# Kernel optimization log

Measured on AMD Instinct MI355X. Metric: run time of the kernel, lower is better.

The kernel has to match this reference:

```python
import jax, jax.numpy as jnp
import numpy as np

H = W = 56
WS = 7            # window size
SHIFT = 3
HEADS = 6
DIM = 192
N = WS * WS       # tokens per window (49)
NW = (H // WS) * (W // WS)  # windows per image (64)
EPS = 1e-5


def _rel_pos_index():
    coords = np.stack(np.meshgrid(np.arange(WS), np.arange(WS), indexing='ij'))
    cf = coords.reshape(2, -1)
    rel = (cf[:, :, None] - cf[:, None, :]).transpose(1, 2, 0)
    rel[:, :, 0] += WS - 1
    rel[:, :, 1] += WS - 1
    rel[:, :, 0] *= 2 * WS - 1
    return rel.sum(-1).astype(np.int32)  # [N, N]


def _attn_mask():
    img = np.zeros([1, H, W, 1], dtype=np.float32)
    slices = (slice(0, -WS), slice(-WS, -SHIFT), slice(-SHIFT, None))
    cnt = 0
    for hs in slices:
        for ws_ in slices:
            img[:, hs, ws_, :] = cnt
            cnt += 1
    m = img.reshape(1, H // WS, WS, W // WS, WS, 1).transpose(0, 1, 3, 2, 4, 5)
    m = m.reshape(-1, N)                      # [nW, N]
    diff = m[:, None, :] - m[:, :, None]
    return np.where(diff != 0, -100.0, 0.0).astype(np.float32)  # [nW, N, N]

_RPI = _rel_pos_index()
_MASK = _attn_mask()


def _ln(x, g, b):
    mu = jnp.mean(x, axis=-1, keepdims=True)
    var = jnp.mean(jnp.square(x - mu), axis=-1, keepdims=True)
    return (x - mu) * jax.lax.rsqrt(var + EPS) * g + b


def setup_inputs() -> dict:
    key = jax.random.key(0)
    ks = jax.random.split(key, 12)
    C, Hd = DIM, DIM * 4
    s = lambda n: 1.0 / np.sqrt(n)
    return {
        'x': jax.random.normal(ks[0], (32, H * W, C), jnp.float32),
        'norm1_g': jnp.ones((C,), jnp.float32),
        'norm1_b': jnp.zeros((C,), jnp.float32),
        'qkv_w': jax.random.normal(ks[1], (C, 3 * C), jnp.float32) * s(C),
        'qkv_b': jnp.zeros((3 * C,), jnp.float32),
        'bias_table': jax.random.normal(ks[2], ((2 * WS - 1) ** 2, HEADS), jnp.float32) * 0.02,
        'proj_w': jax.random.normal(ks[3], (C, C), jnp.float32) * s(C),
        'proj_b': jnp.zeros((C,), jnp.float32),
        'norm2_g': jnp.ones((C,), jnp.float32),
        'norm2_b': jnp.zeros((C,), jnp.float32),
        'fc1_w': jax.random.normal(ks[4], (C, Hd), jnp.float32) * s(C),
        'fc1_b': jnp.zeros((Hd,), jnp.float32),
        'fc2_w': jax.random.normal(ks[5], (Hd, C), jnp.float32) * s(Hd),
        'fc2_b': jnp.zeros((C,), jnp.float32),
    }


def reference(x, norm1_g, norm1_b, qkv_w, qkv_b, bias_table, proj_w, proj_b,
              norm2_g, norm2_b, fc1_w, fc1_b, fc2_w, fc2_b):
    B, L, C = x.shape
    hd = C // HEADS
    scale = hd ** -0.5

    shortcut = x
    h = _ln(x, norm1_g, norm1_b).reshape(B, H, W, C)
    h = jnp.roll(h, (-SHIFT, -SHIFT), axis=(1, 2))

    # window partition -> [B*nW, N, C]
    h = h.reshape(B, H // WS, WS, W // WS, WS, C).transpose(0, 1, 3, 2, 4, 5)
    xw = h.reshape(B * NW, N, C)

    qkv = (xw @ qkv_w + qkv_b).reshape(B * NW, N, 3, HEADS, hd)
    q, k, v = jnp.moveaxis(qkv, 2, 0)                 # each [B*nW, N, H, d]
    q = jnp.swapaxes(q, 1, 2) * scale                 # [B*nW, H, N, d]
    k = jnp.swapaxes(k, 1, 2)
    v = jnp.swapaxes(v, 1, 2)

    attn = jnp.einsum('whnd,whmd->whnm', q, k)        # [B*nW, H, N, N]
    bias = bias_table[jnp.asarray(_RPI).reshape(-1)].reshape(N, N, HEADS)
    attn = attn + jnp.transpose(bias, (2, 0, 1))[None]
    mask = jnp.asarray(_MASK)                         # [nW, N, N]
    attn = attn.reshape(B, NW, HEADS, N, N) + mask[None, :, None]
    attn = jax.nn.softmax(attn.reshape(B * NW, HEADS, N, N), axis=-1)

    out = jnp.einsum('whnm,whmd->whnd', attn, v)      # [B*nW, H, N, d]
    out = jnp.swapaxes(out, 1, 2).reshape(B * NW, N, C)
    out = out @ proj_w + proj_b

    # window reverse -> [B, H, W, C]
    out = out.reshape(B, H // WS, W // WS, WS, WS, C).transpose(0, 1, 3, 2, 4, 5)
    out = out.reshape(B, H, W, C)
    out = jnp.roll(out, (SHIFT, SHIFT), axis=(1, 2)).reshape(B, L, C)

    x = shortcut + out
    hmlp = _ln(x, norm2_g, norm2_b)
    hmlp = jax.nn.gelu(hmlp @ fc1_w + fc1_b, approximate=False) @ fc2_w + fc2_b
    return x + hmlp
```

## Files before the change

### kernel.cpp

```cpp
#include <hip/hip_runtime.h>
#include <hip/hip_bf16.h>
#include <math.h>

static constexpr int CB     = 32;
static constexpr int CH     = 56;
static constexpr int CW     = 56;
static constexpr int CC     = 192;
static constexpr int CSHIFT = 3;
static constexpr int CN     = 49;
static constexpr int CNW    = 64;
static constexpr int CL     = CH * CW;
static constexpr int CM     = CB * CNW * CN;
static constexpr int CHID   = 768;
static constexpr int LN1_BLOCKS  = CM / 4;
static constexpr int PREP_TOTAL  = 110592 + 36864 + 147456 + 147456 + 98304;
static constexpr int PREP_BLOCKS = (PREP_TOTAL + 255) / 256;

typedef __attribute__((ext_vector_type(8))) __bf16 bf16x8;
typedef __attribute__((ext_vector_type(4))) float  f32x4;

__device__ __forceinline__ float bfu2f(unsigned short u) {
  union { unsigned i; float f; } c; c.i = (unsigned)u << 16; return c.f;
}
__device__ __forceinline__ unsigned short f2bu(float f) {
  __hip_bfloat16 b = __float2bfloat16(f);
  return *(unsigned short*)&b;
}
__device__ __forceinline__ float gelu_fast(float v) {
  float e = __expf(-1.702f * v);
  return __fdividef(v, 1.0f + e);
}

#define GLOAD16(g, l) __builtin_amdgcn_global_load_lds( \
    (__attribute__((address_space(1))) void*)(g),       \
    (__attribute__((address_space(3))) void*)(l), 16, 0, 0)

__global__ __launch_bounds__(256)
void ln1_prep_kernel(const float* __restrict__ xin, const float* __restrict__ gamma,
                     const float* __restrict__ beta, __hip_bfloat16* __restrict__ out,
                     const float* __restrict__ qkv_w, const float* __restrict__ proj_w,
                     const float* __restrict__ fc1_w, const float* __restrict__ fc2_w,
                     const float* __restrict__ btab,
                     __hip_bfloat16* __restrict__ wq, __hip_bfloat16* __restrict__ wp,
                     __hip_bfloat16* __restrict__ w1, __hip_bfloat16* __restrict__ w2,
                     float* __restrict__ bias2)
{
  if (blockIdx.x < LN1_BLOCKS) {
    const int wid = threadIdx.x >> 6, lane = threadIdx.x & 63;
    const int m = blockIdx.x * 4 + wid;
    int b   = m / (CNW * CN);
    int rem = m - b * (CNW * CN);
    int nw  = rem / CN, t = rem - nw * CN;
    int wr = nw >> 3, wc = nw & 7;
    int ti = t / 7, tj = t - ti * 7;
    int sr = wr * 7 + ti + CSHIFT; if (sr >= CH) sr -= CH;
    int sc = wc * 7 + tj + CSHIFT; if (sc >= CW) sc -= CW;
    size_t src = ((size_t)b * CL + (size_t)sr * CW + sc) * CC;
    float v0 = xin[src + lane], v1 = xin[src + lane + 64], v2 = xin[src + lane + 128];
    float s  = v0 + v1 + v2;
    float sq = v0 * v0 + v1 * v1 + v2 * v2;
    #pragma unroll
    for (int off = 32; off; off >>= 1) { s += __shfl_xor(s, off); sq += __shfl_xor(sq, off); }
    const float mu  = s * (1.0f / CC);
    const float inv = rsqrtf(sq * (1.0f / CC) - mu * mu + 1e-5f);
    const size_t dst = (size_t)m * CC;
    out[dst + lane      ] = __float2bfloat16((v0 - mu) * inv * gamma[lane      ] + beta[lane      ]);
    out[dst + lane + 64 ] = __float2bfloat16((v1 - mu) * inv * gamma[lane + 64 ] + beta[lane + 64 ]);
    out[dst + lane + 128] = __float2bfloat16((v2 - mu) * inv * gamma[lane + 128] + beta[lane + 128]);
    return;
  }

  int idx = (blockIdx.x - LN1_BLOCKS) * 256 + threadIdx.x;
  if (idx < 110592) {
    int k = idx / 576, n = idx - k * 576;
    wq[n * 192 + k] = __float2bfloat16(qkv_w[idx]);
    return;
  }
  idx -= 110592;
  if (idx < 36864) {
    int k = idx / 192, n = idx - k * 192;
    wp[n * 192 + k] = __float2bfloat16(proj_w[idx]);
    return;
  }
  idx -= 36864;
  if (idx < 147456) {
    int k = idx / 768, n = idx - k * 768;
    w1[n * 192 + k] = __float2bfloat16(fc1_w[idx]);
    return;
  }
  idx -= 147456;
  if (idx < 147456) {
    int k = idx / 192, n = idx - k * 192;
    w2[n * 768 + k] = __float2bfloat16(fc2_w[idx]);
    return;
  }
  idx -= 147456;
  if (idx < 98304) {
    int j = idx & 63, i = (idx >> 6) & 63;
    int rest = idx >> 12;
    int h = rest % 6, wt = rest / 6;
    float val;
    if (i >= 49 || j >= 49) {
      val = -INFINITY;
    } else {
      int ti = i / 7, ci = i - ti * 7;
      int tj = j / 7, cj = j - tj * 7;
      val = btab[((ti - tj + 6) * 13 + (ci - cj + 6)) * 6 + h];
      int hri = (wt & 2) ? ((ti < 4) ? 1 : 2) : 0;
      int hci = (wt & 1) ? ((ci < 4) ? 1 : 2) : 0;
      int hrj = (wt & 2) ? ((tj < 4) ? 1 : 2) : 0;
      int hcj = (wt & 1) ? ((cj < 4) ? 1 : 2) : 0;
      if (hri * 3 + hci != hrj * 3 + hcj) val -= 100.0f;
    }
    bias2[idx] = val;
  }
}

__global__ __launch_bounds__(256)
void ln_kernel(const __hip_bfloat16* __restrict__ xin, const float* __restrict__ gamma,
               const float* __restrict__ beta, __hip_bfloat16* __restrict__ out)
{
  const int wid = threadIdx.x >> 6, lane = threadIdx.x & 63;
  const int m = blockIdx.x * 4 + wid;
  const size_t src = (size_t)m * CC;
  const unsigned short* xb = (const unsigned short*)xin;
  float v0 = bfu2f(xb[src + lane      ]);
  float v1 = bfu2f(xb[src + lane + 64 ]);
  float v2 = bfu2f(xb[src + lane + 128]);
  float s  = v0 + v1 + v2;
  float sq = v0 * v0 + v1 * v1 + v2 * v2;
  #pragma unroll
  for (int off = 32; off; off >>= 1) { s += __shfl_xor(s, off); sq += __shfl_xor(sq, off); }
  const float mu  = s * (1.0f / CC);
  const float inv = rsqrtf(sq * (1.0f / CC) - mu * mu + 1e-5f);
  out[src + lane      ] = __float2bfloat16((v0 - mu) * inv * gamma[lane      ] + beta[lane      ]);
  out[src + lane + 64 ] = __float2bfloat16((v1 - mu) * inv * gamma[lane + 64 ] + beta[lane + 64 ]);
  out[src + lane + 128] = __float2bfloat16((v2 - mu) * inv * gamma[lane + 128] + beta[lane + 128]);
}

template<int K, int N, int BN, int MODE>
__global__ __launch_bounds__(256)
void gemm_mfma(const __hip_bfloat16* __restrict__ Ain, const __hip_bfloat16* __restrict__ Wt,
               const float* __restrict__ bias, void* __restrict__ Outv,
               const void* __restrict__ residv)
{
  constexpr int NT = BN / 32;
  __shared__ short As[128 * 64];
  __shared__ short Bs[BN * 64];

  const int tid  = threadIdx.x;
  const int lane = tid & 63, wid = tid >> 6;

  const int nbx = N / BN;
  const int nwg = nbx * gridDim.y;
  const int wg  = blockIdx.y * nbx + blockIdx.x;
  const int swz = (wg & 7) * (nwg >> 3) + (wg >> 3);
  const int row0 = (swz / nbx) * 128, col0 = (swz % nbx) * BN;

  const int wm = wid >> 1, wn = wid & 1;
  const int lr = lane & 15, lg = lane >> 4;

  const short* A  = (const short*)Ain;
  const short* W  = (const short*)Wt;

  f32x4 acc[4][NT] = {};

  #pragma unroll
  for (int kk = 0; kk < K; kk += 64) {
    #pragma unroll
    for (int it = 0; it < 4; ++it) {
      int c = it * 256 + tid;
      int row = c >> 3, slot = c & 7;
      int kg = (slot ^ (row & 7)) * 8;
      GLOAD16(A + (size_t)(row0 + row) * K + kk + kg, As + c * 8);
    }
    #pragma unroll
    for (int it = 0; it < BN / 32; ++it) {
      int c = it * 256 + tid;
      int row = c >> 3, slot = c & 7;
      int kg = (slot ^ (row & 7)) * 8;
      GLOAD16(W + (size_t)(col0 + row) * K + kk + kg, Bs + c * 8);
    }
    __syncthreads();

    #pragma unroll
    for (int kh = 0; kh < 2; ++kh) {
      const int sb = kh * 4 + lg;
      bf16x8 bfr[NT];
      #pragma unroll
      for (int nt = 0; nt < NT; ++nt) {
        int br = wn * (BN / 2) + nt * 16 + lr;
        bfr[nt] = *(const bf16x8*)(Bs + br * 64 + (sb ^ (br & 7)) * 8);
      }
      #pragma unroll
      for (int m = 0; m < 4; ++m) {
        int ar = wm * 64 + m * 16 + lr;
        bf16x8 afr = *(const bf16x8*)(As + ar * 64 + (sb ^ (ar & 7)) * 8);
        #pragma unroll
        for (int nt = 0; nt < NT; ++nt)
          acc[m][nt] = __builtin_amdgcn_mfma_f32_16x16x32_bf16(afr, bfr[nt], acc[m][nt], 0, 0, 0);
      }
    }
    __syncthreads();
  }

  const int colA = col0 + wn * (BN / 2) + lr;
  float bv[NT];
  #pragma unroll
  for (int nt = 0; nt < NT; ++nt) bv[nt] = bias[colA + nt * 16];

  #pragma unroll
  for (int m = 0; m < 4; ++m) {
    #pragma unroll
    for (int r = 0; r < 4; ++r) {
      const int mrow = row0 + wm * 64 + m * 16 + lg * 4 + r;
      if (MODE == 0) {
        __hip_bfloat16* O = (__hip_bfloat16*)Outv;
        const size_t rr = (size_t)mrow * N + colA;
        #pragma unroll
        for (int nt = 0; nt < NT; ++nt)
          O[rr + nt * 16] = __float2bfloat16(acc[m][nt][r] + bv[nt]);
      } else if (MODE == 4) {
        int b = mrow / (CNW * CN);
        int rem = mrow - b * (CNW * CN);
        int nw = rem / CN, t = rem - nw * CN;
        int wr = nw >> 3, wc = nw & 7;
        int ti = t / 7, tj = t - ti * 7;
        int dr = wr * 7 + ti + CSHIFT; if (dr >= CH) dr -= CH;
        int dc = wc * 7 + tj + CSHIFT; if (dc >= CW) dc -= CW;
        const size_t dst = ((size_t)b * CL + (size_t)dr * CW + dc) * CC + colA;
        const float* resid = (const float*)residv;
        __hip_bfloat16* O = (__hip_bfloat16*)Outv;
        #pragma unroll
        for (int nt = 0; nt < NT; ++nt)
          O[dst + nt * 16] = __float2bfloat16(resid[dst + nt * 16] + acc[m][nt][r] + bv[nt]);
      } else if (MODE == 2) {
        __hip_bfloat16* O = (__hip_bfloat16*)Outv;
        const size_t rr = (size_t)mrow * N + colA;
        #pragma unroll
        for (int nt = 0; nt < NT; ++nt)
          O[rr + nt * 16] = __float2bfloat16(gelu_fast(acc[m][nt][r] + bv[nt]));
      } else {
        float* O = (float*)Outv;
        const unsigned short* resid = (const unsigned short*)residv;
        const size_t rr = (size_t)mrow * N + colA;
        #pragma unroll
        for (int nt = 0; nt < NT; ++nt)
          O[rr + nt * 16] = bfu2f(resid[rr + nt * 16]) + acc[m][nt][r] + bv[nt];
      }
    }
  }
}

__global__ __launch_bounds__(256)
void attn_mfma_kernel(const __hip_bfloat16* __restrict__ qkv,
                      const float* __restrict__ bias2,
                      __hip_bfloat16* __restrict__ attnout)
{
  __shared__ unsigned short VT[4][32 * 72];

  const int wid = threadIdx.x >> 6;
  const int gid = blockIdx.x * 4 + wid;
  const int w = gid / 6, h = gid - (gid / 6) * 6;
  const int lane = threadIdx.x & 63;
  const int lr = lane & 15, lg = lane >> 4;
  const int nw = w & 63;
  const int wt = (((nw >> 3) == 7) ? 2 : 0) + (((nw & 7) == 7) ? 1 : 0);
  const unsigned short* Q = (const unsigned short*)qkv;
  const size_t rowbase = (size_t)w * 49 * 576;
  const float scale = 0.17677669529663687f;
  unsigned short* vt = VT[wid];

  for (int e = lane; e < 196; e += 64) {
    int t = e % 49, c = e / 49;
    uint4 v = *(const uint4*)(Q + rowbase + (size_t)t * 576 + 384 + h * 32 + c * 8);
    unsigned va[4] = {v.x, v.y, v.z, v.w};
    #pragma unroll
    for (int q = 0; q < 4; ++q) {
      vt[(c * 8 + q * 2    ) * 72 + t] = (unsigned short)(va[q] & 0xffff);
      vt[(c * 8 + q * 2 + 1) * 72 + t] = (unsigned short)(va[q] >> 16);
    }
  }
  for (int e = lane; e < 32 * 15; e += 64) {
    int d = e / 15, t = 49 + e - (e / 15) * 15;
    vt[d * 72 + t] = 0;
  }

  bf16x8 qf[4], kf[4];
  #pragma unroll
  for (int it = 0; it < 4; ++it) {
    int tok = it * 16 + lr; if (tok > 48) tok = 48;
    qf[it] = *(const bf16x8*)(Q + rowbase + (size_t)tok * 576 + h * 32 + lg * 8);
  }
  #pragma unroll
  for (int jt = 0; jt < 4; ++jt) {
    int tok = jt * 16 + lr; if (tok > 48) tok = 48;
    kf[jt] = *(const bf16x8*)(Q + rowbase + (size_t)tok * 576 + 192 + h * 32 + lg * 8);
  }

  f32x4 acc[4][4] = {};
  __builtin_amdgcn_s_setprio(1);
  #pragma unroll
  for (int jt = 0; jt < 4; ++jt)
    #pragma unroll
    for (int it = 0; it < 4; ++it)
      acc[jt][it] = __builtin_amdgcn_mfma_f32_16x16x32_bf16(kf[jt], qf[it], acc[jt][it], 0, 0, 0);
  __builtin_amdgcn_s_setprio(0);

  __syncthreads();

  bf16x8 vb[2][2];
  #pragma unroll
  for (int ks = 0; ks < 2; ++ks)
    #pragma unroll
    for (int nt = 0; nt < 2; ++nt)
      vb[ks][nt] = *(const bf16x8*)&vt[(nt * 16 + lr) * 72 + ks * 32 + lg * 8];

  const float* brow = bias2 + ((size_t)(wt * 6 + h) * 64) * 64;
  const int src0 = lr + ((lg & 1) << 5);
  f32x4 o[4][2] = {};

  #pragma unroll
  for (int it = 0; it < 4; ++it) {
    const int i = it * 16 + lr;
    float s[4][4];
    #pragma unroll
    for (int jt = 0; jt < 4; ++jt) {
      float4 bv = *(const float4*)(brow + (size_t)i * 64 + jt * 16 + lg * 4);
      s[jt][0] = fmaf(acc[jt][it][0], scale, bv.x);
      s[jt][1] = fmaf(acc[jt][it][1], scale, bv.y);
      s[jt][2] = fmaf(acc[jt][it][2], scale, bv.z);
      s[jt][3] = fmaf(acc[jt][it][3], scale, bv.w);
    }
    float mx = s[0][0];
    #pragma unroll
    for (int jt = 0; jt < 4; ++jt)
      #pragma unroll
      for (int r = 0; r < 4; ++r) mx = fmaxf(mx, s[jt][r]);
    mx = fmaxf(mx, __shfl_xor(mx, 16));
    mx = fmaxf(mx, __shfl_xor(mx, 32));
    float sum = 0.0f;
    #pragma unroll
    for (int jt = 0; jt < 4; ++jt)
      #pragma unroll
      for (int r = 0; r < 4; ++r) { s[jt][r] = __expf(s[jt][r] - mx); sum += s[jt][r]; }
    sum += __shfl_xor(sum, 16);
    sum += __shfl_xor(sum, 32);
    const float inv = 1.0f / sum;

    unsigned wpk[4][2];
    #pragma unroll
    for (int jt = 0; jt < 4; ++jt) {
      wpk[jt][0] = (unsigned)f2bu(s[jt][0] * inv) | ((unsigned)f2bu(s[jt][1] * inv) << 16);
      wpk[jt][1] = (unsigned)f2bu(s[jt][2] * inv) | ((unsigned)f2bu(s[jt][3] * inv) << 16);
    }
    #pragma unroll
    for (int ks = 0; ks < 2; ++ks) {
      union { bf16x8 v; unsigned u[4]; } pa;
      #pragma unroll
      for (int wd = 0; wd < 4; ++wd) {
        const int src = src0 + ((wd >> 1) << 4);
        unsigned v0 = (unsigned)__shfl((int)wpk[ks * 2    ][wd & 1], src);
        unsigned v1 = (unsigned)__shfl((int)wpk[ks * 2 + 1][wd & 1], src);
        pa.u[wd] = (lg & 2) ? v1 : v0;
      }
      __builtin_amdgcn_s_setprio(1);
      o[it][0] = __builtin_amdgcn_mfma_f32_16x16x32_bf16(pa.v, vb[ks][0], o[it][0], 0, 0, 0);
      o[it][1] = __builtin_amdgcn_mfma_f32_16x16x32_bf16(pa.v, vb[ks][1], o[it][1], 0, 0, 0);
      __builtin_amdgcn_s_setprio(0);
    }
  }

  #pragma unroll
  for (int it = 0; it < 4; ++it) {
    #pragma unroll
    for (int r = 0; r < 4; ++r) {
      int i = it * 16 + lg * 4 + r;
      if (i < 49) {
        size_t dst = ((size_t)w * 49 + i) * 192 + h * 32;
        attnout[dst + lr]      = __float2bfloat16(o[it][0][r]);
        attnout[dst + 16 + lr] = __float2bfloat16(o[it][1][r]);
      }
    }
  }
}

extern "C" void kernel_launch(void* const* d_in, const int* in_sizes, int n_in,
                              void* d_out, int out_size, void* d_ws, size_t ws_size,
                              hipStream_t stream)
{
  const float* x        = (const float*)d_in[0];
  const float* n1g      = (const float*)d_in[1];
  const float* n1b      = (const float*)d_in[2];
  const float* qkv_w    = (const float*)d_in[3];
  const float* qkv_b    = (const float*)d_in[4];
  const float* btab     = (const float*)d_in[5];
  const float* proj_w   = (const float*)d_in[6];
  const float* proj_b   = (const float*)d_in[7];
  const float* n2g      = (const float*)d_in[8];
  const float* n2b      = (const float*)d_in[9];
  const float* fc1_w    = (const float*)d_in[10];
  const float* fc1_b    = (const float*)d_in[11];
  const float* fc2_w    = (const float*)d_in[12];
  const float* fc2_b    = (const float*)d_in[13];
  float* out = (float*)d_out;

  char* ws = (char*)d_ws;
  const size_t szA = (size_t)CM * CC * 2;
  const size_t szB = (size_t)CM * CHID * 2;
  const size_t szW = (size_t)(110592 + 36864 + 147456 + 147456) * 2;
  const size_t szb2 = (size_t)98304 * 4;
  __hip_bfloat16* bufA = (__hip_bfloat16*)ws;
  __hip_bfloat16* bufB = (__hip_bfloat16*)(ws + szA);
  __hip_bfloat16* wq   = (__hip_bfloat16*)(ws + szA + szB);
  __hip_bfloat16* wp   = wq + 576 * 192;
  __hip_bfloat16* w1   = wp + 192 * 192;
  __hip_bfloat16* w2   = w1 + 768 * 192;
  float* bias2         = (float*)(w2 + 192 * 768);
  __hip_bfloat16* bufC = (__hip_bfloat16*)(ws + szA + szB + szW + szb2);


  ln1_prep_kernel<<<LN1_BLOCKS + PREP_BLOCKS, 256, 0, stream>>>(
      x, n1g, n1b, bufA, qkv_w, proj_w, fc1_w, fc2_w, btab, wq, wp, w1, w2, bias2);
  gemm_mfma<192, 576, 96, 0><<<dim3(576 / 96, CM / 128), 256, 0, stream>>>(bufA, wq, qkv_b, bufB, nullptr);
  attn_mfma_kernel<<<2048 * 6 / 4, 256, 0, stream>>>(bufB, bias2, bufA);
  gemm_mfma<192, 192, 64, 4><<<dim3(192 / 64, CM / 128), 256, 0, stream>>>(bufA, wp, proj_b, bufC, x);
  ln_kernel<<<CM / 4, 256, 0, stream>>>(bufC, n2g, n2b, bufA);
  gemm_mfma<192, CHID, 128, 2><<<dim3(CHID / 128, CM / 128), 256, 0, stream>>>(bufA, w1, fc1_b, bufB, nullptr);
  gemm_mfma<CHID, 192, 64, 5><<<dim3(192 / 64, CM / 128), 256, 0, stream>>>(bufB, w2, fc2_b, out, bufC);
}
```

Measured before the change: 308.5 us.

## Fuse QKV projection into window attention kernel, one block per window

Removes the separate QKV GEMM and computes Q, K, V per head inside the attention kernel. Each block handles one window with six waves (one per head), reading the LN1 output and the QKV weights directly. Q and K are staged in LDS, and V is written transposed into the reused Q buffer. This avoids writing and re-reading the bf16 QKV intermediate through global memory. In exchange, each wave re-reads its window's input rows from global or cache for every K-slice, and the weight fetches are not shared across windows, so the MFMA work is less efficient than in a tiled GEMM.

```diff
diff --git a/kernel.cpp b/kernel.cpp
--- a/kernel.cpp
+++ b/kernel.cpp
@@ -214,13 +214,7 @@
     #pragma unroll
     for (int r = 0; r < 4; ++r) {
       const int mrow = row0 + wm * 64 + m * 16 + lg * 4 + r;
-      if (MODE == 0) {
-        __hip_bfloat16* O = (__hip_bfloat16*)Outv;
-        const size_t rr = (size_t)mrow * N + colA;
-        #pragma unroll
-        for (int nt = 0; nt < NT; ++nt)
-          O[rr + nt * 16] = __float2bfloat16(acc[m][nt][r] + bv[nt]);
-      } else if (MODE == 4) {
+      if (MODE == 4) {
         int b = mrow / (CNW * CN);
         int rem = mrow - b * (CNW * CN);
         int nw = rem / CN, t = rem - nw * CN;
@@ -252,62 +246,98 @@
   }
 }
 
-__global__ __launch_bounds__(256)
-void attn_mfma_kernel(const __hip_bfloat16* __restrict__ qkv,
-                      const float* __restrict__ bias2,
-                      __hip_bfloat16* __restrict__ attnout)
+__global__ __launch_bounds__(384)
+void attn_fused_kernel(const unsigned short* __restrict__ xw,
+                       const unsigned short* __restrict__ wq,
+                       const float* __restrict__ qkv_b,
+                       const float* __restrict__ bias2,
+                       __hip_bfloat16* __restrict__ attnout)
 {
-  __shared__ unsigned short VT[4][32 * 72];
-
-  const int wid = threadIdx.x >> 6;
-  const int gid = blockIdx.x * 4 + wid;
-  const int w = gid / 6, h = gid - (gid / 6) * 6;
-  const int lane = threadIdx.x & 63;
+  __shared__ unsigned short QK[6][2][2304];
+
+  const int wid = threadIdx.x >> 6, lane = threadIdx.x & 63;
+  const int w = blockIdx.x, h = wid;
   const int lr = lane & 15, lg = lane >> 4;
   const int nw = w & 63;
   const int wt = (((nw >> 3) == 7) ? 2 : 0) + (((nw & 7) == 7) ? 1 : 0);
-  const unsigned short* Q = (const unsigned short*)qkv;
-  const size_t rowbase = (size_t)w * 49 * 576;
+  const unsigned short* xg = xw + (size_t)w * 49 * 192;
+  unsigned short* q_s = QK[wid][0];
+  unsigned short* k_s = QK[wid][1];
+  unsigned short* vt  = QK[wid][0];
   const float scale = 0.17677669529663687f;
-  unsigned short* vt = VT[wid];
-
-  for (int e = lane; e < 196; e += 64) {
-    int t = e % 49, c = e / 49;
-    uint4 v = *(const uint4*)(Q + rowbase + (size_t)t * 576 + 384 + h * 32 + c * 8);
-    unsigned va[4] = {v.x, v.y, v.z, v.w};
-    #pragma unroll
-    for (int q = 0; q < 4; ++q) {
-      vt[(c * 8 + q * 2    ) * 72 + t] = (unsigned short)(va[q] & 0xffff);
-      vt[(c * 8 + q * 2 + 1) * 72 + t] = (unsigned short)(va[q] >> 16);
-    }
-  }
-  for (int e = lane; e < 32 * 15; e += 64) {
-    int d = e / 15, t = 49 + e - (e / 15) * 15;
-    vt[d * 72 + t] = 0;
+
+  #pragma unroll
+  for (int op = 0; op < 2; ++op) {
+    f32x4 a4[4][2] = {};
+    #pragma unroll
+    for (int ksl = 0; ksl < 6; ++ksl) {
+      bf16x8 bfr[2];
+      #pragma unroll
+      for (int nt = 0; nt < 2; ++nt)
+        bfr[nt] = *(const bf16x8*)(wq + (size_t)(op * 192 + h * 32 + nt * 16 + lr) * 192 + ksl * 32 + lg * 8);
+      #pragma unroll
+      for (int it = 0; it < 4; ++it) {
+        int tok = it * 16 + lr; if (tok > 48) tok = 48;
+        bf16x8 af = *(const bf16x8*)(xg + (size_t)tok * 192 + ksl * 32 + lg * 8);
+        a4[it][0] = __builtin_amdgcn_mfma_f32_16x16x32_bf16(af, bfr[0], a4[it][0], 0, 0, 0);
+        a4[it][1] = __builtin_amdgcn_mfma_f32_16x16x32_bf16(af, bfr[1], a4[it][1], 0, 0, 0);
+      }
+    }
+    unsigned short* dst = op ? k_s : q_s;
+    #pragma unroll
+    for (int nt = 0; nt < 2; ++nt) {
+      const float bb = qkv_b[op * 192 + h * 32 + nt * 16 + lr];
+      #pragma unroll
+      for (int it = 0; it < 4; ++it)
+        #pragma unroll
+        for (int r = 0; r < 4; ++r)
+          dst[(it * 16 + lg * 4 + r) * 36 + nt * 16 + lr] = f2bu(a4[it][nt][r] + bb);
+    }
   }
 
   bf16x8 qf[4], kf[4];
   #pragma unroll
-  for (int it = 0; it < 4; ++it) {
-    int tok = it * 16 + lr; if (tok > 48) tok = 48;
-    qf[it] = *(const bf16x8*)(Q + rowbase + (size_t)tok * 576 + h * 32 + lg * 8);
-  }
-  #pragma unroll
-  for (int jt = 0; jt < 4; ++jt) {
-    int tok = jt * 16 + lr; if (tok > 48) tok = 48;
-    kf[jt] = *(const bf16x8*)(Q + rowbase + (size_t)tok * 576 + 192 + h * 32 + lg * 8);
-  }
-
-  f32x4 acc[4][4] = {};
+  for (int it = 0; it < 4; ++it)
+    qf[it] = *(const bf16x8*)&q_s[(it * 16 + lr) * 36 + lg * 8];
+  #pragma unroll
+  for (int jt = 0; jt < 4; ++jt)
+    kf[jt] = *(const bf16x8*)&k_s[(jt * 16 + lr) * 36 + lg * 8];
+
+  f32x4 accs[4][4] = {};
   __builtin_amdgcn_s_setprio(1);
   #pragma unroll
   for (int jt = 0; jt < 4; ++jt)
     #pragma unroll
     for (int it = 0; it < 4; ++it)
-      acc[jt][it] = __builtin_amdgcn_mfma_f32_16x16x32_bf16(kf[jt], qf[it], acc[jt][it], 0, 0, 0);
+      accs[jt][it] = __builtin_amdgcn_mfma_f32_16x16x32_bf16(kf[jt], qf[it], accs[jt][it], 0, 0, 0);
   __builtin_amdgcn_s_setprio(0);
 
-  __syncthreads();
+  {
+    f32x4 a4[4][2] = {};
+    #pragma unroll
+    for (int ksl = 0; ksl < 6; ++ksl) {
+      bf16x8 bfr[2];
+      #pragma unroll
+      for (int nt = 0; nt < 2; ++nt)
+        bfr[nt] = *(const bf16x8*)(wq + (size_t)(384 + h * 32 + nt * 16 + lr) * 192 + ksl * 32 + lg * 8);
+      #pragma unroll
+      for (int it = 0; it < 4; ++it) {
+        int tok = it * 16 + lr; if (tok > 48) tok = 48;
+        bf16x8 af = *(const bf16x8*)(xg + (size_t)tok * 192 + ksl * 32 + lg * 8);
+        a4[it][0] = __builtin_amdgcn_mfma_f32_16x16x32_bf16(af, bfr[0], a4[it][0], 0, 0, 0);
+        a4[it][1] = __builtin_amdgcn_mfma_f32_16x16x32_bf16(af, bfr[1], a4[it][1], 0, 0, 0);
+      }
+    }
+    #pragma unroll
+    for (int nt = 0; nt < 2; ++nt) {
+      const float bb = qkv_b[384 + h * 32 + nt * 16 + lr];
+      #pragma unroll
+      for (int it = 0; it < 4; ++it)
+        #pragma unroll
+        for (int r = 0; r < 4; ++r)
+          vt[(nt * 16 + lr) * 72 + it * 16 + lg * 4 + r] = f2bu(a4[it][nt][r] + bb);
+    }
+  }
 
   bf16x8 vb[2][2];
   #pragma unroll
@@ -327,10 +357,10 @@
     #pragma unroll
     for (int jt = 0; jt < 4; ++jt) {
       float4 bv = *(const float4*)(brow + (size_t)i * 64 + jt * 16 + lg * 4);
-      s[jt][0] = fmaf(acc[jt][it][0], scale, bv.x);
-      s[jt][1] = fmaf(acc[jt][it][1], scale, bv.y);
-      s[jt][2] = fmaf(acc[jt][it][2], scale, bv.z);
-      s[jt][3] = fmaf(acc[jt][it][3], scale, bv.w);
+      s[jt][0] = fmaf(accs[jt][it][0], scale, bv.x);
+      s[jt][1] = fmaf(accs[jt][it][1], scale, bv.y);
+      s[jt][2] = fmaf(accs[jt][it][2], scale, bv.z);
+      s[jt][3] = fmaf(accs[jt][it][3], scale, bv.w);
     }
     float mx = s[0][0];
     #pragma unroll
@@ -419,12 +449,11 @@
   float* bias2         = (float*)(w2 + 192 * 768);
   __hip_bfloat16* bufC = (__hip_bfloat16*)(ws + szA + szB + szW + szb2);
 
-
   ln1_prep_kernel<<<LN1_BLOCKS + PREP_BLOCKS, 256, 0, stream>>>(
       x, n1g, n1b, bufA, qkv_w, proj_w, fc1_w, fc2_w, btab, wq, wp, w1, w2, bias2);
-  gemm_mfma<192, 576, 96, 0><<<dim3(576 / 96, CM / 128), 256, 0, stream>>>(bufA, wq, qkv_b, bufB, nullptr);
-  attn_mfma_kernel<<<2048 * 6 / 4, 256, 0, stream>>>(bufB, bias2, bufA);
-  gemm_mfma<192, 192, 64, 4><<<dim3(192 / 64, CM / 128), 256, 0, stream>>>(bufA, wp, proj_b, bufC, x);
+  attn_fused_kernel<<<CB * CNW, 384, 0, stream>>>(
+      (const unsigned short*)bufA, (const unsigned short*)wq, qkv_b, bias2, bufB);
+  gemm_mfma<192, 192, 64, 4><<<dim3(192 / 64, CM / 128), 256, 0, stream>>>(bufB, wp, proj_b, bufC, x);
   ln_kernel<<<CM / 4, 256, 0, stream>>>(bufC, n2g, n2b, bufA);
   gemm_mfma<192, CHID, 128, 2><<<dim3(CHID / 128, CM / 128), 256, 0, stream>>>(bufA, w1, fc1_b, bufB, nullptr);
   gemm_mfma<CHID, 192, 64, 5><<<dim3(192 / 64, CM / 128), 256, 0, stream>>>(bufB, w2, fc2_b, out, bufC);
```

Result: slower. 399.3 us (+29.4%).
